# Kernel optimization log

Hardware: AMD Instinct MI355X
Metric: run time of the kernel (lower is better)

The kernel has to match this reference:

```python
import jax, jax.numpy as jnp
import numpy as np

# Base model: 2-layer ReLU MLP, D->H->O, state flattened as [w1, b1, w2, b2]
D, H, O = 32, 64, 1
T = 1024          # xtype_size (number of tickers)
M = 8             # mesa_parameter_size
N = 32768         # rows
S = H * D + H + O * H + O  # 2177, flattened state size


def setup_inputs() -> dict:
    key = jax.random.key(0)
    ks = jax.random.split(key, 6)
    x = jax.random.normal(ks[0], (N, D), dtype=jnp.float32)
    ticker = jax.random.randint(ks[1], (N,), 0, T, dtype=jnp.int32)
    mesa_layer_weight = jax.random.uniform(ks[2], (M, T), jnp.float32, -0.1, 0.1)
    meta_layer_weight = jax.random.uniform(ks[3], (S, M), jnp.float32, -0.1, 0.1)
    meta_layer_bias = jnp.zeros((S,), jnp.float32)
    base_state = jax.random.normal(ks[4], (S,), dtype=jnp.float32) * 0.05
    return {"x": x, "ticker": ticker,
            "mesa_layer_weight": mesa_layer_weight,
            "meta_layer_weight": meta_layer_weight,
            "meta_layer_bias": meta_layer_bias,
            "base_state": base_state}


def _unflatten(states):
    # states: [T, S] -> per-ticker MLP params
    i0 = H * D
    i1 = i0 + H
    i2 = i1 + O * H
    w1 = states[:, :i0].reshape(T, H, D)
    b1 = states[:, i0:i1]                  # [T, H]
    w2 = states[:, i1:i2].reshape(T, O, H)
    b2 = states[:, i2:]                    # [T, O]
    return w1, b1, w2, b2


def reference(x, ticker, mesa_layer_weight, meta_layer_weight, meta_layer_bias, base_state):
    # F.linear(one_hot_i, mesa_W) selects column i -> all mesa states = mesa_W.T : [T, M]
    # temp = meta_W @ mesa_state for every ticker at once: [T, S]
    temps = jnp.einsum('mt,sm->ts', mesa_layer_weight, meta_layer_weight)
    # allow_meta mask is all-ones (allow_meta_structure=None); dropout p=0 is identity
    states = base_state[None, :] + meta_layer_bias[None, :] + temps  # [T, S]
    w1, b1, w2, b2 = _unflatten(states)
    # gather per-row ticker params and run the base MLP forward
    h = jax.nn.relu(jnp.einsum('nd,nhd->nh', x, w1[ticker]) + b1[ticker])  # [N, H]
    out = jnp.einsum('nh,noh->no', h, w2[ticker]) + b2[ticker]             # [N, O]
    return out
```

## Files before the change

kernel.cpp:

```cpp
#include <hip/hip_runtime.h>

#define DD 32
#define HH 64
#define TT 1024
#define MM 8
#define NN 32768
#define SS 2177
#define SP 2180

__global__ __launch_bounds__(256) void states_kernel(
    const float* __restrict__ mesa,
    const float* __restrict__ metaw,
    const float* __restrict__ metab,
    const float* __restrict__ base,
    float* __restrict__ states)
{
    int s = blockIdx.x * 256 + threadIdx.x;
    int t = blockIdx.y;
    if (s >= SS) return;
    const float4* mw = (const float4*)(metaw + s * MM);
    float4 a = mw[0], b = mw[1];
    float acc = base[s] + metab[s];
    acc = fmaf(a.x, mesa[0 * TT + t], acc);
    acc = fmaf(a.y, mesa[1 * TT + t], acc);
    acc = fmaf(a.z, mesa[2 * TT + t], acc);
    acc = fmaf(a.w, mesa[3 * TT + t], acc);
    acc = fmaf(b.x, mesa[4 * TT + t], acc);
    acc = fmaf(b.y, mesa[5 * TT + t], acc);
    acc = fmaf(b.z, mesa[6 * TT + t], acc);
    acc = fmaf(b.w, mesa[7 * TT + t], acc);
    states[(size_t)t * SP + s] = acc;
}

__global__ __launch_bounds__(256) void mlp_kernel(
    const float* __restrict__ x,
    const int*   __restrict__ ticker,
    const float* __restrict__ states,
    float* __restrict__ out)
{
    int wave = threadIdx.x >> 6;
    int lane = threadIdx.x & 63;
    int n = blockIdx.x * 4 + wave;

    int t = ticker[n];
    const float* row = states + (size_t)t * SP;

    float xv = (lane < DD) ? x[n * DD + lane] : 0.0f;

    const float4* wp = (const float4*)(row + lane * DD);
    float h = 0.0f;
#pragma unroll
    for (int q = 0; q < 8; ++q) {
        float4 w = wp[q];
        h = fmaf(__shfl(xv, 4 * q + 0, 64), w.x, h);
        h = fmaf(__shfl(xv, 4 * q + 1, 64), w.y, h);
        h = fmaf(__shfl(xv, 4 * q + 2, 64), w.z, h);
        h = fmaf(__shfl(xv, 4 * q + 3, 64), w.w, h);
    }
    h += row[HH * DD + lane];
    h = fmaxf(h, 0.0f);

    float p = h * row[HH * DD + HH + lane];
#pragma unroll
    for (int off = 32; off >= 1; off >>= 1)
        p += __shfl_down(p, off, 64);

    if (lane == 0)
        out[n] = p + row[HH * DD + HH + HH];
}

extern "C" void kernel_launch(void* const* d_in, const int* in_sizes, int n_in,
                              void* d_out, int out_size, void* d_ws, size_t ws_size,
                              hipStream_t stream) {
    const float* x      = (const float*)d_in[0];
    const int*   ticker = (const int*)  d_in[1];
    const float* mesa   = (const float*)d_in[2];
    const float* metaw  = (const float*)d_in[3];
    const float* metab  = (const float*)d_in[4];
    const float* base   = (const float*)d_in[5];
    float* out    = (float*)d_out;
    float* states = (float*)d_ws;

    dim3 g1((SS + 255) / 256, TT);
    states_kernel<<<g1, 256, 0, stream>>>(mesa, metaw, metab, base, states);

    mlp_kernel<<<NN / 4, 256, 0, stream>>>(x, ticker, states, out);
}
```

Before: 106.7 us.

## Sort rows by ticker via counting sort so blocks reuse per-ticker weights

```diff
diff --git a/kernel.cpp b/kernel.cpp
--- a/kernel.cpp
+++ b/kernel.cpp
@@ -7,6 +7,45 @@
 #define NN 32768
 #define SS 2177
 #define SP 2180
+
+#define WS_COUNTS 0
+#define WS_CURSOR 4096
+#define WS_PERM   8192
+#define WS_STATES 139264
+
+__global__ __launch_bounds__(256) void hist_kernel(
+    const int* __restrict__ ticker, int* __restrict__ counts)
+{
+    int n = blockIdx.x * 256 + threadIdx.x;
+    atomicAdd(&counts[ticker[n]], 1);
+}
+
+__global__ __launch_bounds__(1024) void scan_kernel(
+    const int* __restrict__ counts, int* __restrict__ cursor)
+{
+    __shared__ int sc[TT];
+    int tid = threadIdx.x;
+    int c = counts[tid];
+    sc[tid] = c;
+    __syncthreads();
+#pragma unroll
+    for (int off = 1; off < TT; off <<= 1) {
+        int v = (tid >= off) ? sc[tid - off] : 0;
+        __syncthreads();
+        sc[tid] += v;
+        __syncthreads();
+    }
+    cursor[tid] = sc[tid] - c;
+}
+
+__global__ __launch_bounds__(256) void scatter_kernel(
+    const int* __restrict__ ticker, int* __restrict__ cursor, int* __restrict__ perm)
+{
+    int n = blockIdx.x * 256 + threadIdx.x;
+    int t = ticker[n];
+    int pos = atomicAdd(&cursor[t], 1);
+    perm[pos] = n;
+}
 
 __global__ __launch_bounds__(256) void states_kernel(
     const float* __restrict__ mesa,
@@ -32,16 +71,18 @@
     states[(size_t)t * SP + s] = acc;
 }
 
-__global__ __launch_bounds__(256) void mlp_kernel(
+__global__ __launch_bounds__(1024) void mlp_kernel(
     const float* __restrict__ x,
     const int*   __restrict__ ticker,
+    const int*   __restrict__ perm,
     const float* __restrict__ states,
     float* __restrict__ out)
 {
     int wave = threadIdx.x >> 6;
     int lane = threadIdx.x & 63;
-    int n = blockIdx.x * 4 + wave;
+    int idx = blockIdx.x * 16 + wave;
 
+    int n = perm[idx];
     int t = ticker[n];
     const float* row = states + (size_t)t * SP;
 
@@ -78,11 +119,21 @@
     const float* metaw  = (const float*)d_in[3];
     const float* metab  = (const float*)d_in[4];
     const float* base   = (const float*)d_in[5];
-    float* out    = (float*)d_out;
-    float* states = (float*)d_ws;
+    float* out = (float*)d_out;
+
+    char* ws = (char*)d_ws;
+    int*   counts = (int*)(ws + WS_COUNTS);
+    int*   cursor = (int*)(ws + WS_CURSOR);
+    int*   perm   = (int*)(ws + WS_PERM);
+    float* states = (float*)(ws + WS_STATES);
+
+    hipMemsetAsync(counts, 0, TT * sizeof(int), stream);
+    hist_kernel<<<NN / 256, 256, 0, stream>>>(ticker, counts);
+    scan_kernel<<<1, 1024, 0, stream>>>(counts, cursor);
+    scatter_kernel<<<NN / 256, 256, 0, stream>>>(ticker, cursor, perm);
 
     dim3 g1((SS + 255) / 256, TT);
     states_kernel<<<g1, 256, 0, stream>>>(mesa, metaw, metab, base, states);
 
-    mlp_kernel<<<NN / 4, 256, 0, stream>>>(x, ticker, states, out);
+    mlp_kernel<<<NN / 16, 1024, 0, stream>>>(x, ticker, perm, states, out);
 }
```

Result: slower. 127.7 us (+19.6%).

## Fuse state construction into MLP via low-rank algebraic refactoring

Applied to the files above, without the earlier changes.

```diff
diff --git a/kernel.cpp b/kernel.cpp
--- a/kernel.cpp
+++ b/kernel.cpp
@@ -1,72 +1,133 @@
 #include <hip/hip_runtime.h>
 
+
 #define DD 32
-#define HH 64
 #define TT 1024
 #define MM 8
-#define NN 32768
-#define SS 2177
-#define SP 2180
+#define KB 8
 
-__global__ __launch_bounds__(256) void states_kernel(
+__global__ __launch_bounds__(1024, 4) void fused_kernel(
+    const float* __restrict__ x,
+    const int*   __restrict__ ticker,
     const float* __restrict__ mesa,
     const float* __restrict__ metaw,
     const float* __restrict__ metab,
     const float* __restrict__ base,
-    float* __restrict__ states)
-{
-    int s = blockIdx.x * 256 + threadIdx.x;
-    int t = blockIdx.y;
-    if (s >= SS) return;
-    const float4* mw = (const float4*)(metaw + s * MM);
-    float4 a = mw[0], b = mw[1];
-    float acc = base[s] + metab[s];
-    acc = fmaf(a.x, mesa[0 * TT + t], acc);
-    acc = fmaf(a.y, mesa[1 * TT + t], acc);
-    acc = fmaf(a.z, mesa[2 * TT + t], acc);
-    acc = fmaf(a.w, mesa[3 * TT + t], acc);
-    acc = fmaf(b.x, mesa[4 * TT + t], acc);
-    acc = fmaf(b.y, mesa[5 * TT + t], acc);
-    acc = fmaf(b.z, mesa[6 * TT + t], acc);
-    acc = fmaf(b.w, mesa[7 * TT + t], acc);
-    states[(size_t)t * SP + s] = acc;
-}
-
-__global__ __launch_bounds__(256) void mlp_kernel(
-    const float* __restrict__ x,
-    const int*   __restrict__ ticker,
-    const float* __restrict__ states,
     float* __restrict__ out)
 {
-    int wave = threadIdx.x >> 6;
-    int lane = threadIdx.x & 63;
-    int n = blockIdx.x * 4 + wave;
+    __shared__ float4 U4[32 * 2 * 64];
+    __shared__ float4 B1q[8 * 64];
+    __shared__ float4 Ub1[2 * 64];
+    __shared__ float4 U2q[2 * 64];
+    __shared__ float  B1b[64];
+    __shared__ float  B2b[64];
 
-    int t = ticker[n];
-    const float* row = states + (size_t)t * SP;
+    const int tid  = threadIdx.x;
+    const int lane = tid & 63;
+    const int dm   = tid >> 6;
 
-    float xv = (lane < DD) ? x[n * DD + lane] : 0.0f;
+    #pragma unroll
+    for (int i2 = 0; i2 < 4; ++i2) {
+        int idx = dm * 4 + i2;
+        int d = idx >> 1, m4 = idx & 1;
+        U4[(d * 2 + m4) * 64 + lane] =
+            *(const float4*)(metaw + ((lane * 32 + d) * MM + m4 * 4));
+    }
+    if (dm < 8) {
+        int s0 = lane * 32 + dm * 4;
+        float4 bv = *(const float4*)(base  + s0);
+        float4 mv = *(const float4*)(metab + s0);
+        B1q[dm * 64 + lane] = make_float4(bv.x + mv.x, bv.y + mv.y, bv.z + mv.z, bv.w + mv.w);
+    } else if (dm < 10) {
+        int m4 = dm - 8;
+        Ub1[m4 * 64 + lane] = *(const float4*)(metaw + ((2048 + lane) * MM + m4 * 4));
+    } else if (dm < 12) {
+        int m4 = dm - 10;
+        U2q[m4 * 64 + lane] = *(const float4*)(metaw + ((2112 + lane) * MM + m4 * 4));
+    } else if (dm == 12) {
+        B1b[lane] = base[2048 + lane] + metab[2048 + lane];
+    } else if (dm == 13) {
+        B2b[lane] = base[2112 + lane] + metab[2112 + lane];
+    }
+    __syncthreads();
 
-    const float4* wp = (const float4*)(row + lane * DD);
-    float h = 0.0f;
-#pragma unroll
-    for (int q = 0; q < 8; ++q) {
-        float4 w = wp[q];
-        h = fmaf(__shfl(xv, 4 * q + 0, 64), w.x, h);
-        h = fmaf(__shfl(xv, 4 * q + 1, 64), w.y, h);
-        h = fmaf(__shfl(xv, 4 * q + 2, 64), w.z, h);
-        h = fmaf(__shfl(xv, 4 * q + 3, 64), w.w, h);
+    const int n0 = blockIdx.x * 128 + dm * KB;
+
+    float xr[4];
+    #pragma unroll
+    for (int r = 0; r < 4; ++r) xr[r] = x[n0 * DD + r * 64 + lane];
+
+    float4 g0[KB], g1[KB];
+    float  c0[KB];
+    #pragma unroll
+    for (int i = 0; i < KB; ++i) {
+        g0[i] = make_float4(0.f, 0.f, 0.f, 0.f);
+        g1[i] = make_float4(0.f, 0.f, 0.f, 0.f);
+        c0[i] = 0.f;
     }
-    h += row[HH * DD + lane];
-    h = fmaxf(h, 0.0f);
 
-    float p = h * row[HH * DD + HH + lane];
-#pragma unroll
-    for (int off = 32; off >= 1; off >>= 1)
-        p += __shfl_down(p, off, 64);
+    for (int dq = 0; dq < 8; ++dq) {
+        float4 bq = B1q[dq * 64 + lane];
+        #pragma unroll
+        for (int dd = 0; dd < 4; ++dd) {
+            int d = dq * 4 + dd;
+            float4 u0 = U4[(d * 2 + 0) * 64 + lane];
+            float4 u1 = U4[(d * 2 + 1) * 64 + lane];
+            float bs = (dd == 0) ? bq.x : (dd == 1) ? bq.y : (dd == 2) ? bq.z : bq.w;
+            #pragma unroll
+            for (int i = 0; i < KB; ++i) {
+                int lidx = (i & 1) * 32 + d;
+                float xv = __uint_as_float(
+                    __builtin_amdgcn_readlane(__float_as_uint(xr[i >> 1]), lidx));
+                c0[i]   = fmaf(xv, bs,   c0[i]);
+                g0[i].x = fmaf(xv, u0.x, g0[i].x);
+                g0[i].y = fmaf(xv, u0.y, g0[i].y);
+                g0[i].z = fmaf(xv, u0.z, g0[i].z);
+                g0[i].w = fmaf(xv, u0.w, g0[i].w);
+                g1[i].x = fmaf(xv, u1.x, g1[i].x);
+                g1[i].y = fmaf(xv, u1.y, g1[i].y);
+                g1[i].z = fmaf(xv, u1.z, g1[i].z);
+                g1[i].w = fmaf(xv, u1.w, g1[i].w);
+            }
+        }
+    }
 
-    if (lane == 0)
-        out[n] = p + row[HH * DD + HH + HH];
+    float4 ub1a = Ub1[0 * 64 + lane], ub1b = Ub1[1 * 64 + lane];
+    float4 u2a  = U2q[0 * 64 + lane], u2b  = U2q[1 * 64 + lane];
+    float  b1base = B1b[lane], b2base = B2b[lane];
+    float4 w2m0 = *(const float4*)(metaw + 2176 * MM);
+    float4 w2m1 = *(const float4*)(metaw + 2176 * MM + 4);
+    float  b2c  = base[2176] + metab[2176];
+
+    #pragma unroll
+    for (int i = 0; i < KB; ++i) {
+        int n = n0 + i;
+        int t = ticker[n];
+        float mi[8];
+        #pragma unroll
+        for (int m = 0; m < 8; ++m) mi[m] = mesa[m * TT + t];
+
+        float b1 = b1base
+                 + mi[0] * ub1a.x + mi[1] * ub1a.y + mi[2] * ub1a.z + mi[3] * ub1a.w
+                 + mi[4] * ub1b.x + mi[5] * ub1b.y + mi[6] * ub1b.z + mi[7] * ub1b.w;
+        float h = c0[i] + b1
+                 + mi[0] * g0[i].x + mi[1] * g0[i].y + mi[2] * g0[i].z + mi[3] * g0[i].w
+                 + mi[4] * g1[i].x + mi[5] * g1[i].y + mi[6] * g1[i].z + mi[7] * g1[i].w;
+        h = fmaxf(h, 0.f);
+        float w2 = b2base
+                 + mi[0] * u2a.x + mi[1] * u2a.y + mi[2] * u2a.z + mi[3] * u2a.w
+                 + mi[4] * u2b.x + mi[5] * u2b.y + mi[6] * u2b.z + mi[7] * u2b.w;
+        float p = h * w2;
+        #pragma unroll
+        for (int off = 32; off >= 1; off >>= 1)
+            p += __shfl_down(p, off, 64);
+        if (lane == 0) {
+            float b2 = b2c
+                 + mi[0] * w2m0.x + mi[1] * w2m0.y + mi[2] * w2m0.z + mi[3] * w2m0.w
+                 + mi[4] * w2m1.x + mi[5] * w2m1.y + mi[6] * w2m1.z + mi[7] * w2m1.w;
+            out[n] = p + b2;
+        }
+    }
 }
 
 extern "C" void kernel_launch(void* const* d_in, const int* in_sizes, int n_in,
@@ -78,11 +139,7 @@
     const float* metaw  = (const float*)d_in[3];
     const float* metab  = (const float*)d_in[4];
     const float* base   = (const float*)d_in[5];
-    float* out    = (float*)d_out;
-    float* states = (float*)d_ws;
+    float* out = (float*)d_out;
 
-    dim3 g1((SS + 255) / 256, TT);
-    states_kernel<<<g1, 256, 0, stream>>>(mesa, metaw, metab, base, states);
-
-    mlp_kernel<<<NN / 4, 256, 0, stream>>>(x, ticker, states, out);
+    fused_kernel<<<256, 1024, 0, stream>>>(x, ticker, mesa, metaw, metab, base, out);
 }
```

Measured after the change: 86.86 us. 1.23x faster.
